# Performance work log

Measured on AMD Instinct MI355X. Metric: run time of the kernel, lower is better.

Reference implementation:

```python
import jax, jax.numpy as jnp
import numpy as np

B, P, L = 1024, 20, 3          # batch pairs, paths per pair, path length
T = L + 2                      # LSTM sequence length (news1 + path + news2)
E = 128                        # embedding_size (compressed / LSTM hidden)
D_DOC = 768                    # doc_embedding_size
D_ENT = 100                    # entity_embedding_size
N_DOC, N_ENT, N_REL = 50000, 200000, 60
GAMMA = 2.0
EPS = 1e-7


def setup_inputs() -> dict:
    key = jax.random.key(0)
    ks = jax.random.split(key, 24)
    s = lambda fan_in: 1.0 / np.sqrt(fan_in)
    u = lambda k, shape, sc: jax.random.uniform(k, shape, jnp.float32, -sc, sc)
    return {
        "item1": jax.random.randint(ks[0], (B,), 0, N_DOC),
        "item2": jax.random.randint(ks[1], (B,), 0, N_DOC),
        "paths": jax.random.randint(ks[2], (B, P, L), 0, N_ENT),
        "edges": jax.random.randint(ks[3], (B, P, L), 0, N_REL),
        "label": jnp.round(jax.random.uniform(ks[4], (B,), jnp.float32)),
        # embedding tables (frozen pretrained in the original)
        "doc_table": jax.random.normal(ks[5], (N_DOC, D_DOC), jnp.float32),
        "entity_table": jax.random.normal(ks[6], (N_ENT, D_ENT), jnp.float32),
        "relation_table": jax.random.normal(ks[7], (N_REL, D_ENT), jnp.float32),
        # news_compress: Linear(D_DOC,E) -> ELU -> Linear(E,E) -> Tanh
        "nc_W1": u(ks[8], (D_DOC, E), s(D_DOC)), "nc_b1": u(ks[9], (E,), s(D_DOC)),
        "nc_W2": u(ks[10], (E, E), s(E)),        "nc_b2": u(ks[11], (E,), s(E)),
        # entity / relation compress: Linear(D_ENT,E) -> Tanh
        "ec_W": u(ks[12], (D_ENT, E), s(D_ENT)), "ec_b": u(ks[13], (E,), s(D_ENT)),
        "rc_W": u(ks[14], (D_ENT, E), s(D_ENT)), "rc_b": u(ks[15], (E,), s(D_ENT)),
        # LSTM(input=2E, hidden=E); torch gate order i,f,g,o
        "W_ih": u(ks[16], (4 * E, 2 * E), s(E)), "W_hh": u(ks[17], (4 * E, E), s(E)),
        "b_ih": u(ks[18], (4 * E,), s(E)),       "b_hh": u(ks[19], (4 * E,), s(E)),
        # mlp: Linear(E,E) -> ReLU -> Linear(E,1)
        "mlp_W1": u(ks[20], (E, E), s(E)), "mlp_b1": u(ks[21], (E,), s(E)),
        "mlp_W2": u(ks[22], (E, 1), s(E)), "mlp_b2": u(ks[23], (1,), s(E)),
    }


def _lstm_last(x, W_ih, W_hh, b_ih, b_hh):
    # x: [N, T, 2E] -> last hidden state [N, E]
    N = x.shape[0]
    H = W_hh.shape[1]
    b = b_ih + b_hh

    def step(carry, xt):
        h, c = carry
        gates = xt @ W_ih.T + h @ W_hh.T + b          # [N, 4H]
        i, f, g, o = jnp.split(gates, 4, axis=-1)
        c = jax.nn.sigmoid(f) * c + jax.nn.sigmoid(i) * jnp.tanh(g)
        h = jax.nn.sigmoid(o) * jnp.tanh(c)
        return (h, c), None

    init = (jnp.zeros((N, H), x.dtype), jnp.zeros((N, H), x.dtype))
    (h, _), _ = jax.lax.scan(step, init, jnp.swapaxes(x, 0, 1))  # scan over T
    return h


def reference(item1, item2, paths, edges, label,
              doc_table, entity_table, relation_table,
              nc_W1, nc_b1, nc_W2, nc_b2, ec_W, ec_b, rc_W, rc_b,
              W_ih, W_hh, b_ih, b_hh, mlp_W1, mlp_b1, mlp_W2, mlp_b2):
    news_compress = lambda d: jnp.tanh(jax.nn.elu(d @ nc_W1 + nc_b1) @ nc_W2 + nc_b2)
    news1 = news_compress(doc_table[item1])               # [B, E]
    news2 = news_compress(doc_table[item2])               # [B, E]

    node_emb = jnp.tanh(entity_table[paths] @ ec_W + ec_b)          # [B,P,L,E]
    edge_ids = jnp.concatenate([edges, jnp.zeros((B, P, 2), edges.dtype)], axis=-1)  # edge+[0,0]
    rel_emb = jnp.tanh(relation_table[edge_ids] @ rc_W + rc_b)      # [B,P,T,E]

    n1 = jnp.broadcast_to(news1[:, None, None, :], (B, P, 1, E))
    n2 = jnp.broadcast_to(news2[:, None, None, :], (B, P, 1, E))
    nodes_seq = jnp.concatenate([n1, node_emb, n2], axis=2)         # [B,P,T,E]
    lstm_in = jnp.concatenate([nodes_seq, rel_emb], axis=-1)        # [B,P,T,2E]

    h_last = _lstm_last(lstm_in.reshape(B * P, T, 2 * E), W_ih, W_hh, b_ih, b_hh)
    scores = (jax.nn.relu(h_last @ mlp_W1 + mlp_b1) @ mlp_W2 + mlp_b2).reshape(B, P)

    predicts = jax.nn.sigmoid(jax.nn.logsumexp(scores / GAMMA, axis=1))  # [B]
    p = jnp.clip(predicts, EPS, 1.0 - EPS)
    loss = -jnp.mean(label * jnp.log(p) + (1.0 - label) * jnp.log(1.0 - p))
    return loss, predicts, scores
```

## Files before the change

### kernel.cpp

```cpp
#include <hip/hip_runtime.h>
#include <hip/hip_bf16.h>

#define B_  1024
#define P_  20
#define L_  3
#define T_  5
#define E_  128
#define N_  (B_*P_)
#define DDOC 768
#define DENT 100
#define XROWS 124929

typedef unsigned short u16;
typedef unsigned int   u32;
typedef __attribute__((ext_vector_type(8))) __bf16 bf16x8;
typedef __attribute__((ext_vector_type(4))) float  f32x4;

__device__ __forceinline__ float sigmoidf_(float x) { return 1.f / (1.f + expf(-x)); }
__device__ __forceinline__ u16 f2bf_rne(float x) {
    u32 b = __float_as_uint(x);
    b += 0x7fffu + ((b >> 16) & 1u);
    return (u16)(b >> 16);
}
__device__ __forceinline__ float bf2f(u16 u) { return __uint_as_float(((u32)u) << 16); }
__device__ __forceinline__ u32 pack2(u16 a, u16 b) { return (u32)a | ((u32)b << 16); }

__global__ __launch_bounds__(256) void news_kernel(
    const int* __restrict__ item1, const int* __restrict__ item2,
    const float* __restrict__ doc_table,
    const float* __restrict__ W1, const float* __restrict__ b1,
    const float* __restrict__ W2, const float* __restrict__ b2,
    u16* __restrict__ xh, u16* __restrict__ xl)
{
    __shared__ float d_lds[8][DDOC];
    __shared__ float h1_lds[8][132];
    const int tid = threadIdx.x;
    const int row0 = blockIdx.x * 8;

    for (int i = tid; i < 8 * 192; i += 256) {
        int r = i / 192, q = i % 192;
        int gr = row0 + r;
        int id = (gr < B_) ? item1[gr] : item2[gr - B_];
        reinterpret_cast<float4*>(&d_lds[r][0])[q] =
            reinterpret_cast<const float4*>(doc_table + (size_t)id * DDOC)[q];
    }
    __syncthreads();

    const int tn = tid & 127;
    const int tm = tid >> 7;
    float acc[4];
#pragma unroll
    for (int r = 0; r < 4; r++) acc[r] = b1[tn];

    for (int k = 0; k < DDOC; k += 4) {
        float w0 = W1[(k + 0) * 128 + tn];
        float w1 = W1[(k + 1) * 128 + tn];
        float w2 = W1[(k + 2) * 128 + tn];
        float w3 = W1[(k + 3) * 128 + tn];
#pragma unroll
        for (int r = 0; r < 4; r++) {
            const float4 dv = *reinterpret_cast<const float4*>(&d_lds[tm * 4 + r][k]);
            acc[r] = fmaf(dv.x, w0, acc[r]);
            acc[r] = fmaf(dv.y, w1, acc[r]);
            acc[r] = fmaf(dv.z, w2, acc[r]);
            acc[r] = fmaf(dv.w, w3, acc[r]);
        }
    }
#pragma unroll
    for (int r = 0; r < 4; r++) {
        float v = acc[r];
        h1_lds[tm * 4 + r][tn] = (v > 0.f) ? v : expm1f(v);
    }
    __syncthreads();

    float acc2[4];
#pragma unroll
    for (int r = 0; r < 4; r++) acc2[r] = b2[tn];
    for (int k = 0; k < 128; k += 4) {
        float w0 = W2[(k + 0) * 128 + tn];
        float w1 = W2[(k + 1) * 128 + tn];
        float w2 = W2[(k + 2) * 128 + tn];
        float w3 = W2[(k + 3) * 128 + tn];
#pragma unroll
        for (int r = 0; r < 4; r++) {
            const float4 hv = *reinterpret_cast<const float4*>(&h1_lds[tm * 4 + r][k]);
            acc2[r] = fmaf(hv.x, w0, acc2[r]);
            acc2[r] = fmaf(hv.y, w1, acc2[r]);
            acc2[r] = fmaf(hv.z, w2, acc2[r]);
            acc2[r] = fmaf(hv.w, w3, acc2[r]);
        }
    }
#pragma unroll
    for (int r = 0; r < 4; r++) {
        float v = tanhf(acc2[r]);
        size_t off = (size_t)(row0 + tm * 4 + r) * 128 + tn;
        u16 hh = f2bf_rne(v);
        xh[off] = hh;
        xl[off] = f2bf_rne(v - bf2f(hh));
    }
}

__global__ __launch_bounds__(256) void compress_kernel(
    const int* __restrict__ paths, const int* __restrict__ edges,
    const float* __restrict__ entity_table, const float* __restrict__ relation_table,
    const float* __restrict__ ec_W, const float* __restrict__ ec_b,
    const float* __restrict__ rc_W, const float* __restrict__ rc_b,
    u16* __restrict__ xh, u16* __restrict__ xl)
{
    __shared__ float w_lds[DENT][128];
    __shared__ float x_lds[32][104];
    __shared__ int idx_lds[32];

    const int tid = threadIdx.x;
    const int bid = blockIdx.x;
    const bool is_ent  = (bid < 1920);
    const bool is_rel0 = (bid == 3840);
    const float* W     = is_ent ? ec_W : rc_W;
    const float* bias  = is_ent ? ec_b : rc_b;
    const float* table = is_ent ? entity_table : relation_table;
    int nrows; int row0; int xbase;
    if (is_ent)        { row0 = bid * 32;          nrows = 32; xbase = 2048; }
    else if (!is_rel0) { row0 = (bid - 1920) * 32; nrows = 32; xbase = 63488; }
    else               { row0 = 0;                 nrows = 1;  xbase = 124928; }

    for (int i = tid; i < 3200; i += 256)
        reinterpret_cast<float4*>(&w_lds[0][0])[i] = reinterpret_cast<const float4*>(W)[i];
    if (tid < nrows) {
        int gr = row0 + tid;
        idx_lds[tid] = is_rel0 ? 0 : (is_ent ? paths[gr] : edges[gr]);
    }
    __syncthreads();

    for (int i = tid; i < nrows * 25; i += 256) {
        int r = i / 25, q = i % 25;
        reinterpret_cast<float4*>(&x_lds[r][0])[q] =
            reinterpret_cast<const float4*>(table + (size_t)idx_lds[r] * DENT)[q];
    }
    __syncthreads();

    const int tn = tid & 31;
    const int tm = tid >> 5;
    float acc[4][4];
#pragma unroll
    for (int ri = 0; ri < 4; ri++)
#pragma unroll
        for (int cj = 0; cj < 4; cj++) acc[ri][cj] = bias[tn * 4 + cj];

    for (int k = 0; k < DENT; k += 4) {
        float4 wv[4];
#pragma unroll
        for (int kk = 0; kk < 4; kk++)
            wv[kk] = *reinterpret_cast<const float4*>(&w_lds[k + kk][tn * 4]);
#pragma unroll
        for (int ri = 0; ri < 4; ri++) {
            const float4 xv = *reinterpret_cast<const float4*>(&x_lds[tm * 4 + ri][k]);
            float xs[4] = {xv.x, xv.y, xv.z, xv.w};
#pragma unroll
            for (int kk = 0; kk < 4; kk++) {
                acc[ri][0] = fmaf(xs[kk], wv[kk].x, acc[ri][0]);
                acc[ri][1] = fmaf(xs[kk], wv[kk].y, acc[ri][1]);
                acc[ri][2] = fmaf(xs[kk], wv[kk].z, acc[ri][2]);
                acc[ri][3] = fmaf(xs[kk], wv[kk].w, acc[ri][3]);
            }
        }
    }
#pragma unroll
    for (int ri = 0; ri < 4; ri++) {
        int r = tm * 4 + ri;
        if (r < nrows) {
            size_t xrow = (size_t)(xbase + row0 + r);
            u16 hh[4], ll[4];
#pragma unroll
            for (int cj = 0; cj < 4; cj++) {
                float v = tanhf(acc[ri][cj]);
                hh[cj] = f2bf_rne(v);
                ll[cj] = f2bf_rne(v - bf2f(hh[cj]));
            }
            uint2 oh, ol;
            oh.x = pack2(hh[0], hh[1]); oh.y = pack2(hh[2], hh[3]);
            ol.x = pack2(ll[0], ll[1]); ol.y = pack2(ll[2], ll[3]);
            *reinterpret_cast<uint2*>(&xh[xrow * 128 + tn * 4]) = oh;
            *reinterpret_cast<uint2*>(&xl[xrow * 128 + tn * 4]) = ol;
        }
    }
}

__global__ __launch_bounds__(256) void split_w_kernel(
    const float* __restrict__ W_ih, const float* __restrict__ W_hh,
    u16* __restrict__ wih_h, u16* __restrict__ wih_l,
    u16* __restrict__ whh_h, u16* __restrict__ whh_l)
{
    int i = blockIdx.x * 256 + threadIdx.x;
    if (i < 512 * 256) {
        float w = W_ih[i];
        u16 h = f2bf_rne(w);
        wih_h[i] = h; wih_l[i] = f2bf_rne(w - bf2f(h));
    } else {
        int j = i - 512 * 256;
        float w = W_hh[j];
        u16 h = f2bf_rne(w);
        whh_h[j] = h; whh_l[j] = f2bf_rne(w - bf2f(h));
    }
}

__global__ __launch_bounds__(256) void lstm_gemm(
    int t,
    const u16* __restrict__ xh, const u16* __restrict__ xl,
    const u16* __restrict__ wih_h, const u16* __restrict__ wih_l,
    const u16* __restrict__ whh_h, const u16* __restrict__ whh_l,
    const u16* __restrict__ h_hi, const u16* __restrict__ h_lo,
    float* __restrict__ gbuf)
{
    __shared__ u16 a_h[128 * 40], a_l[128 * 40], b_h[128 * 40], b_l[128 * 40];
    __shared__ int nrow[128], rrow[128];

    const int tid  = threadIdx.x;
    const int rb   = blockIdx.x >> 2;
    const int cb   = blockIdx.x & 3;
    const int row0 = rb * 128;
    const int gate0 = cb * 128;

    if (tid < 128) {
        int n = row0 + tid;
        int nr;
        if (t == 0)      nr = n / P_;
        else if (t == 4) nr = 1024 + n / P_;
        else             nr = 2048 + n * 3 + (t - 1);
        nrow[tid] = nr;
        rrow[tid] = (t < 3) ? (63488 + n * 3 + t) : 124928;
    }

    f32x4 acc[4][4];
#pragma unroll
    for (int rg = 0; rg < 4; rg++)
#pragma unroll
        for (int cg = 0; cg < 4; cg++)
            acc[rg][cg] = (f32x4){0.f, 0.f, 0.f, 0.f};

    const int ln   = tid & 63;
    const int wv   = tid >> 6;
    const int wrow = (wv >> 1) * 64;
    const int wcol = (wv & 1) * 64;
    const int l15  = ln & 15;
    const int lk   = (ln >> 4) * 8;

    const int nch = (t == 0) ? 8 : 12;
    __syncthreads();

    for (int ch = 0; ch < nch; ch++) {
        const int k0 = ch * 32;
        for (int i = tid; i < 2048; i += 256) {
            const int ab = i >> 10;
            const int pl = (i >> 9) & 1;
            const int r  = (i >> 2) & 127;
            const int q  = i & 3;
            const u16* src;
            if (ab == 0) {
                if (k0 < 128)
                    src = (pl ? xl : xh) + (size_t)nrow[r] * 128 + k0 + q * 8;
                else if (k0 < 256)
                    src = (pl ? xl : xh) + (size_t)rrow[r] * 128 + (k0 - 128) + q * 8;
                else
                    src = (pl ? h_lo : h_hi) + (size_t)(row0 + r) * 128 + (k0 - 256) + q * 8;
            } else {
                if (k0 < 256)
                    src = (pl ? wih_l : wih_h) + (size_t)(gate0 + r) * 256 + k0 + q * 8;
                else
                    src = (pl ? whh_l : whh_h) + (size_t)(gate0 + r) * 128 + (k0 - 256) + q * 8;
            }
            u16* dst = (ab ? (pl ? b_l : b_h) : (pl ? a_l : a_h)) + r * 40 + q * 8;
            *reinterpret_cast<uint4*>(dst) = *reinterpret_cast<const uint4*>(src);
        }
        __syncthreads();

        bf16x8 ah[4], al[4], bh[4], bl[4];
#pragma unroll
        for (int g = 0; g < 4; g++) {
            const int ao = (wrow + g * 16 + l15) * 40 + lk;
            ah[g] = *reinterpret_cast<const bf16x8*>(&a_h[ao]);
            al[g] = *reinterpret_cast<const bf16x8*>(&a_l[ao]);
            const int bo = (wcol + g * 16 + l15) * 40 + lk;
            bh[g] = *reinterpret_cast<const bf16x8*>(&b_h[bo]);
            bl[g] = *reinterpret_cast<const bf16x8*>(&b_l[bo]);
        }
#pragma unroll
        for (int rg = 0; rg < 4; rg++)
#pragma unroll
            for (int cg = 0; cg < 4; cg++) {
                acc[rg][cg] = __builtin_amdgcn_mfma_f32_16x16x32_bf16(ah[rg], bh[cg], acc[rg][cg], 0, 0, 0);
                acc[rg][cg] = __builtin_amdgcn_mfma_f32_16x16x32_bf16(al[rg], bh[cg], acc[rg][cg], 0, 0, 0);
                acc[rg][cg] = __builtin_amdgcn_mfma_f32_16x16x32_bf16(ah[rg], bl[cg], acc[rg][cg], 0, 0, 0);
            }
        __syncthreads();
    }

#pragma unroll
    for (int rg = 0; rg < 4; rg++)
#pragma unroll
        for (int cg = 0; cg < 4; cg++) {
            const int col = gate0 + wcol + cg * 16 + l15;
#pragma unroll
            for (int e = 0; e < 4; e++) {
                const int row = row0 + wrow + rg * 16 + (ln >> 4) * 4 + e;
                gbuf[(size_t)row * 512 + col] = acc[rg][cg][e];
            }
        }
}

__global__ __launch_bounds__(256) void cell_kernel(
    int t,
    const float* __restrict__ gbuf,
    const float* __restrict__ b_ih, const float* __restrict__ b_hh,
    float* __restrict__ cbuf,
    u16* __restrict__ h_hi, u16* __restrict__ h_lo)
{
    const int idx = blockIdx.x * 256 + threadIdx.x;
    const int n  = idx >> 7;
    const int hd = idx & 127;
    const size_t base = (size_t)n * 512 + hd;
    float gi = gbuf[base +   0] + b_ih[hd +   0] + b_hh[hd +   0];
    float gf = gbuf[base + 128] + b_ih[hd + 128] + b_hh[hd + 128];
    float gg = gbuf[base + 256] + b_ih[hd + 256] + b_hh[hd + 256];
    float go = gbuf[base + 384] + b_ih[hd + 384] + b_hh[hd + 384];
    float cp = (t == 0) ? 0.f : cbuf[idx];
    float cn = sigmoidf_(gf) * cp + sigmoidf_(gi) * tanhf(gg);
    cbuf[idx] = cn;
    float hn = sigmoidf_(go) * tanhf(cn);
    u16 hh = f2bf_rne(hn);
    h_hi[idx] = hh;
    h_lo[idx] = f2bf_rne(hn - bf2f(hh));
}

__global__ __launch_bounds__(256) void mlp_kernel(
    const u16* __restrict__ h_hi, const u16* __restrict__ h_lo,
    const float* __restrict__ W1, const float* __restrict__ b1,
    const float* __restrict__ W2, const float* __restrict__ b2,
    float* __restrict__ scores)
{
    __shared__ float h_lds[16][132];
    __shared__ float z_lds[16][132];
    const int tid = threadIdx.x;
    const int row0 = blockIdx.x * 16;

    {
        const int r = tid >> 4, q = tid & 15;
        const size_t off = (size_t)(row0 + r) * 128 + q * 8;
        uint4 vh = *reinterpret_cast<const uint4*>(&h_hi[off]);
        uint4 vl = *reinterpret_cast<const uint4*>(&h_lo[off]);
        const u16* sh = reinterpret_cast<const u16*>(&vh);
        const u16* sl = reinterpret_cast<const u16*>(&vl);
#pragma unroll
        for (int e = 0; e < 8; e++)
            h_lds[r][q * 8 + e] = bf2f(sh[e]) + bf2f(sl[e]);
    }
    __syncthreads();

    const int tn = tid & 127;
    const int tm = tid >> 7;
    float acc[8];
#pragma unroll
    for (int r = 0; r < 8; r++) acc[r] = b1[tn];
    for (int k = 0; k < 128; k += 4) {
        float w0 = W1[(k + 0) * 128 + tn];
        float w1 = W1[(k + 1) * 128 + tn];
        float w2 = W1[(k + 2) * 128 + tn];
        float w3 = W1[(k + 3) * 128 + tn];
#pragma unroll
        for (int r = 0; r < 8; r++) {
            const float4 hv = *reinterpret_cast<const float4*>(&h_lds[tm * 8 + r][k]);
            acc[r] = fmaf(hv.x, w0, acc[r]);
            acc[r] = fmaf(hv.y, w1, acc[r]);
            acc[r] = fmaf(hv.z, w2, acc[r]);
            acc[r] = fmaf(hv.w, w3, acc[r]);
        }
    }
#pragma unroll
    for (int r = 0; r < 8; r++)
        z_lds[tm * 8 + r][tn] = fmaxf(acc[r], 0.f);
    __syncthreads();

    const int row = tid >> 4;
    const int part = tid & 15;
    float s = 0.f;
#pragma unroll
    for (int i = 0; i < 8; i++) {
        int j = part + i * 16;
        s += z_lds[row][j] * W2[j];
    }
    s += __shfl_xor(s, 8, 16);
    s += __shfl_xor(s, 4, 16);
    s += __shfl_xor(s, 2, 16);
    s += __shfl_xor(s, 1, 16);
    if (part == 0)
        scores[row0 + row] = s + b2[0];
}

__global__ __launch_bounds__(1024) void final_kernel(
    const float* __restrict__ label, const float* scores, float* out)
{
    __shared__ float red[1024];
    const int b = threadIdx.x;
    const float* s = scores + (size_t)b * P_;
    float m = -1e30f;
#pragma unroll
    for (int p = 0; p < P_; p++) m = fmaxf(m, s[p] * 0.5f);
    float sum = 0.f;
#pragma unroll
    for (int p = 0; p < P_; p++) sum += expf(s[p] * 0.5f - m);
    float lse = m + logf(sum);
    float pr = 1.f / (1.f + expf(-lse));
    out[1 + b] = pr;
    float pc = fminf(fmaxf(pr, 1e-7f), 1.f - 1e-7f);
    float lb = label[b];
    red[b] = -(lb * logf(pc) + (1.f - lb) * logf(1.f - pc));
    __syncthreads();
    for (int st = 512; st > 0; st >>= 1) {
        if (b < st) red[b] += red[b + st];
        __syncthreads();
    }
    if (b == 0) out[0] = red[0] * (1.f / 1024.f);
}

extern "C" void kernel_launch(void* const* d_in, const int* in_sizes, int n_in,
                              void* d_out, int out_size, void* d_ws, size_t ws_size,
                              hipStream_t stream)
{
    const int*   item1     = (const int*)  d_in[0];
    const int*   item2     = (const int*)  d_in[1];
    const int*   paths     = (const int*)  d_in[2];
    const int*   edges     = (const int*)  d_in[3];
    const float* label     = (const float*)d_in[4];
    const float* doc_table = (const float*)d_in[5];
    const float* ent_table = (const float*)d_in[6];
    const float* rel_table = (const float*)d_in[7];
    const float* nc_W1     = (const float*)d_in[8];
    const float* nc_b1     = (const float*)d_in[9];
    const float* nc_W2     = (const float*)d_in[10];
    const float* nc_b2     = (const float*)d_in[11];
    const float* ec_W      = (const float*)d_in[12];
    const float* ec_b      = (const float*)d_in[13];
    const float* rc_W      = (const float*)d_in[14];
    const float* rc_b      = (const float*)d_in[15];
    const float* W_ih      = (const float*)d_in[16];
    const float* W_hh      = (const float*)d_in[17];
    const float* b_ih      = (const float*)d_in[18];
    const float* b_hh      = (const float*)d_in[19];
    const float* mlp_W1    = (const float*)d_in[20];
    const float* mlp_b1    = (const float*)d_in[21];
    const float* mlp_W2    = (const float*)d_in[22];
    const float* mlp_b2    = (const float*)d_in[23];

    char* p = (char*)d_ws;
    u16* xh    = (u16*)p;  p += (size_t)XROWS * 128 * 2;
    u16* xl    = (u16*)p;  p += (size_t)XROWS * 128 * 2;
    u16* wih_h = (u16*)p;  p += 512 * 256 * 2;
    u16* wih_l = (u16*)p;  p += 512 * 256 * 2;
    u16* whh_h = (u16*)p;  p += 512 * 128 * 2;
    u16* whh_l = (u16*)p;  p += 512 * 128 * 2;
    float* gbuf = (float*)p; p += (size_t)N_ * 512 * 4;
    float* cbuf = (float*)p; p += (size_t)N_ * 128 * 4;
    u16* h_hi  = (u16*)p;  p += (size_t)N_ * 128 * 2;
    u16* h_lo  = (u16*)p;  p += (size_t)N_ * 128 * 2;

    float* out    = (float*)d_out;
    float* scores = out + 1 + B_;

    news_kernel<<<256, 256, 0, stream>>>(item1, item2, doc_table,
                                         nc_W1, nc_b1, nc_W2, nc_b2, xh, xl);
    compress_kernel<<<3841, 256, 0, stream>>>(paths, edges, ent_table, rel_table,
                                              ec_W, ec_b, rc_W, rc_b, xh, xl);
    split_w_kernel<<<768, 256, 0, stream>>>(W_ih, W_hh, wih_h, wih_l, whh_h, whh_l);

    for (int t = 0; t < T_; t++) {
        lstm_gemm<<<640, 256, 0, stream>>>(t, xh, xl, wih_h, wih_l, whh_h, whh_l,
                                           h_hi, h_lo, gbuf);
        cell_kernel<<<N_ * 128 / 256, 256, 0, stream>>>(t, gbuf, b_ih, b_hh,
                                                        cbuf, h_hi, h_lo);
    }
    mlp_kernel<<<1280, 256, 0, stream>>>(h_hi, h_lo, mlp_W1, mlp_b1, mlp_W2, mlp_b2, scores);
    final_kernel<<<1, 1024, 0, stream>>>(label, scores, out);
}
```

Baseline: 715.4 us.

## Compress relation table once, MFMA entity compress, async double-buffered LSTM GEMM loads

Relation embeddings are now compressed only for the 60 distinct relation ids, and the LSTM GEMM gathers them through the edge indices. This replaces the per-path relation rows and shrinks the x buffer. Entity compression moves from scalar FP32 FMAs to split-bf16 MFMA, using transposed weights prepared in a merged prep kernel. The LSTM GEMM now loads tiles straight from global memory into XOR-swizzled LDS with double buffering and explicit waitcnt/barrier control, so loads overlap with MFMA work. The hand-placed waitcnt and barrier ordering raises the risk of subtle synchronisation bugs.

```diff
diff --git a/kernel.cpp b/kernel.cpp
--- a/kernel.cpp
+++ b/kernel.cpp
@@ -9,7 +9,9 @@
 #define N_  (B_*P_)
 #define DDOC 768
 #define DENT 100
-#define XROWS 124929
+#define NODE_BASE 2048
+#define RELC_BASE 63488
+#define XROWS 63548
 
 typedef unsigned short u16;
 typedef unsigned int   u32;
@@ -24,6 +26,12 @@
 }
 __device__ __forceinline__ float bf2f(u16 u) { return __uint_as_float(((u32)u) << 16); }
 __device__ __forceinline__ u32 pack2(u16 a, u16 b) { return (u32)a | ((u32)b << 16); }
+
+__device__ __forceinline__ void gl2lds16(const void* g, void* l) {
+    __builtin_amdgcn_global_load_lds(
+        (const __attribute__((address_space(1))) void*)g,
+        (__attribute__((address_space(3))) void*)l, 16, 0, 0);
+}
 
 __global__ __launch_bounds__(256) void news_kernel(
     const int* __restrict__ item1, const int* __restrict__ item2,
@@ -100,106 +108,183 @@
     }
 }
 
-__global__ __launch_bounds__(256) void compress_kernel(
-    const int* __restrict__ paths, const int* __restrict__ edges,
-    const float* __restrict__ entity_table, const float* __restrict__ relation_table,
-    const float* __restrict__ ec_W, const float* __restrict__ ec_b,
-    const float* __restrict__ rc_W, const float* __restrict__ rc_b,
-    u16* __restrict__ xh, u16* __restrict__ xl)
-{
-    __shared__ float w_lds[DENT][128];
-    __shared__ float x_lds[32][104];
-    __shared__ int idx_lds[32];
-
-    const int tid = threadIdx.x;
-    const int bid = blockIdx.x;
-    const bool is_ent  = (bid < 1920);
-    const bool is_rel0 = (bid == 3840);
-    const float* W     = is_ent ? ec_W : rc_W;
-    const float* bias  = is_ent ? ec_b : rc_b;
-    const float* table = is_ent ? entity_table : relation_table;
-    int nrows; int row0; int xbase;
-    if (is_ent)        { row0 = bid * 32;          nrows = 32; xbase = 2048; }
-    else if (!is_rel0) { row0 = (bid - 1920) * 32; nrows = 32; xbase = 63488; }
-    else               { row0 = 0;                 nrows = 1;  xbase = 124928; }
-
-    for (int i = tid; i < 3200; i += 256)
-        reinterpret_cast<float4*>(&w_lds[0][0])[i] = reinterpret_cast<const float4*>(W)[i];
-    if (tid < nrows) {
-        int gr = row0 + tid;
-        idx_lds[tid] = is_rel0 ? 0 : (is_ent ? paths[gr] : edges[gr]);
-    }
-    __syncthreads();
-
-    for (int i = tid; i < nrows * 25; i += 256) {
-        int r = i / 25, q = i % 25;
-        reinterpret_cast<float4*>(&x_lds[r][0])[q] =
-            reinterpret_cast<const float4*>(table + (size_t)idx_lds[r] * DENT)[q];
-    }
-    __syncthreads();
-
-    const int tn = tid & 31;
-    const int tm = tid >> 5;
-    float acc[4][4];
-#pragma unroll
-    for (int ri = 0; ri < 4; ri++)
-#pragma unroll
-        for (int cj = 0; cj < 4; cj++) acc[ri][cj] = bias[tn * 4 + cj];
-
-    for (int k = 0; k < DENT; k += 4) {
-        float4 wv[4];
-#pragma unroll
-        for (int kk = 0; kk < 4; kk++)
-            wv[kk] = *reinterpret_cast<const float4*>(&w_lds[k + kk][tn * 4]);
-#pragma unroll
-        for (int ri = 0; ri < 4; ri++) {
-            const float4 xv = *reinterpret_cast<const float4*>(&x_lds[tm * 4 + ri][k]);
-            float xs[4] = {xv.x, xv.y, xv.z, xv.w};
-#pragma unroll
-            for (int kk = 0; kk < 4; kk++) {
-                acc[ri][0] = fmaf(xs[kk], wv[kk].x, acc[ri][0]);
-                acc[ri][1] = fmaf(xs[kk], wv[kk].y, acc[ri][1]);
-                acc[ri][2] = fmaf(xs[kk], wv[kk].z, acc[ri][2]);
-                acc[ri][3] = fmaf(xs[kk], wv[kk].w, acc[ri][3]);
-            }
-        }
-    }
-#pragma unroll
-    for (int ri = 0; ri < 4; ri++) {
-        int r = tm * 4 + ri;
-        if (r < nrows) {
-            size_t xrow = (size_t)(xbase + row0 + r);
-            u16 hh[4], ll[4];
-#pragma unroll
-            for (int cj = 0; cj < 4; cj++) {
-                float v = tanhf(acc[ri][cj]);
-                hh[cj] = f2bf_rne(v);
-                ll[cj] = f2bf_rne(v - bf2f(hh[cj]));
-            }
-            uint2 oh, ol;
-            oh.x = pack2(hh[0], hh[1]); oh.y = pack2(hh[2], hh[3]);
-            ol.x = pack2(ll[0], ll[1]); ol.y = pack2(ll[2], ll[3]);
-            *reinterpret_cast<uint2*>(&xh[xrow * 128 + tn * 4]) = oh;
-            *reinterpret_cast<uint2*>(&xl[xrow * 128 + tn * 4]) = ol;
-        }
-    }
-}
-
-__global__ __launch_bounds__(256) void split_w_kernel(
+__global__ __launch_bounds__(256) void prep_kernel(
     const float* __restrict__ W_ih, const float* __restrict__ W_hh,
+    const float* __restrict__ ec_W, const float* __restrict__ rc_W,
     u16* __restrict__ wih_h, u16* __restrict__ wih_l,
-    u16* __restrict__ whh_h, u16* __restrict__ whh_l)
+    u16* __restrict__ whh_h, u16* __restrict__ whh_l,
+    u16* __restrict__ ecwt_h, u16* __restrict__ ecwt_l,
+    u16* __restrict__ rcwt_h, u16* __restrict__ rcwt_l)
 {
     int i = blockIdx.x * 256 + threadIdx.x;
-    if (i < 512 * 256) {
+    if (i < 131072) {
         float w = W_ih[i];
         u16 h = f2bf_rne(w);
         wih_h[i] = h; wih_l[i] = f2bf_rne(w - bf2f(h));
-    } else {
-        int j = i - 512 * 256;
+    } else if (i < 196608) {
+        int j = i - 131072;
         float w = W_hh[j];
         u16 h = f2bf_rne(w);
         whh_h[j] = h; whh_l[j] = f2bf_rne(w - bf2f(h));
+    } else if (i < 212992) {
+        int j = i - 196608;
+        int col = j & 127, k = j >> 7;
+        float w = (k < DENT) ? ec_W[k * 128 + col] : 0.f;
+        u16 h = f2bf_rne(w);
+        ecwt_h[col * 128 + k] = h; ecwt_l[col * 128 + k] = f2bf_rne(w - bf2f(h));
+    } else {
+        int j = i - 212992;
+        int col = j & 127, k = j >> 7;
+        float w = (k < DENT) ? rc_W[k * 128 + col] : 0.f;
+        u16 h = f2bf_rne(w);
+        rcwt_h[col * 128 + k] = h; rcwt_l[col * 128 + k] = f2bf_rne(w - bf2f(h));
+    }
+}
+
+__global__ __launch_bounds__(256) void compress_mfma(
+    const int* __restrict__ paths,
+    const float* __restrict__ entity_table, const float* __restrict__ relation_table,
+    const u16* __restrict__ ecwt_h, const u16* __restrict__ ecwt_l,
+    const u16* __restrict__ rcwt_h, const u16* __restrict__ rcwt_l,
+    const float* __restrict__ ec_b, const float* __restrict__ rc_b,
+    u16* __restrict__ xh, u16* __restrict__ xl)
+{
+    __shared__ char lds_raw[65536];
+    u16* a_lds = (u16*)lds_raw;
+    u16* b_lds = (u16*)(lds_raw + 18432);
+    u32* o_lds = (u32*)lds_raw;
+
+    const int tid = threadIdx.x;
+    const int bid = blockIdx.x;
+    const bool is_rel = (bid == 480);
+    const int r0 = bid * 128;
+    const u16* wth = is_rel ? rcwt_h : ecwt_h;
+    const u16* wtl = is_rel ? rcwt_l : ecwt_l;
+    const float* bias = is_rel ? rc_b : ec_b;
+    const float* table = is_rel ? relation_table : entity_table;
+
+    const int ar = tid >> 1, ahalf = tid & 1;
+    int gidx;
+    if (is_rel) gidx = (ar < 60) ? ar : 0;
+    else        gidx = paths[r0 + ar];
+    const float* arow = table + (size_t)gidx * DENT;
+
+    const int ln = tid & 63, wv = tid >> 6;
+    const int wrow = (wv >> 1) * 64, wcol = (wv & 1) * 64;
+    const int l15 = ln & 15, lq = ln >> 4;
+
+    f32x4 acc[4][4];
+#pragma unroll
+    for (int cg = 0; cg < 4; cg++) {
+        float bv = bias[wcol + cg * 16 + l15];
+#pragma unroll
+        for (int rg = 0; rg < 4; rg++)
+            acc[rg][cg] = (f32x4){bv, bv, bv, bv};
+    }
+
+    for (int c = 0; c < 4; ++c) {
+        {
+            float v[16];
+#pragma unroll
+            for (int q = 0; q < 4; ++q) {
+                int kq = c * 32 + ahalf * 16 + q * 4;
+                float4 f = (kq < DENT) ? *reinterpret_cast<const float4*>(arow + kq)
+                                       : make_float4(0.f, 0.f, 0.f, 0.f);
+                v[q * 4 + 0] = f.x; v[q * 4 + 1] = f.y;
+                v[q * 4 + 2] = f.z; v[q * 4 + 3] = f.w;
+            }
+            u16 hh[16], llo[16];
+#pragma unroll
+            for (int e = 0; e < 16; ++e) {
+                hh[e] = f2bf_rne(v[e]);
+                llo[e] = f2bf_rne(v[e] - bf2f(hh[e]));
+            }
+            u16* ap = a_lds + ar * 72;
+            uint4 o0, o1, o2, o3;
+            o0.x = pack2(hh[0], hh[1]);  o0.y = pack2(hh[2], hh[3]);
+            o0.z = pack2(hh[4], hh[5]);  o0.w = pack2(hh[6], hh[7]);
+            o1.x = pack2(hh[8], hh[9]);  o1.y = pack2(hh[10], hh[11]);
+            o1.z = pack2(hh[12], hh[13]); o1.w = pack2(hh[14], hh[15]);
+            o2.x = pack2(llo[0], llo[1]);  o2.y = pack2(llo[2], llo[3]);
+            o2.z = pack2(llo[4], llo[5]);  o2.w = pack2(llo[6], llo[7]);
+            o3.x = pack2(llo[8], llo[9]);  o3.y = pack2(llo[10], llo[11]);
+            o3.z = pack2(llo[12], llo[13]); o3.w = pack2(llo[14], llo[15]);
+            *reinterpret_cast<uint4*>(ap + ahalf * 16 + 0) = o0;
+            *reinterpret_cast<uint4*>(ap + ahalf * 16 + 8) = o1;
+            *reinterpret_cast<uint4*>(ap + 32 + ahalf * 16 + 0) = o2;
+            *reinterpret_cast<uint4*>(ap + 32 + ahalf * 16 + 8) = o3;
+        }
+#pragma unroll
+        for (int i = 0; i < 4; ++i) {
+            int idx = tid + i * 256;
+            int br = idx >> 3, s = idx & 7;
+            const u16* src = ((s & 4) ? wtl : wth) + br * 128 + c * 32 + (s & 3) * 8;
+            *reinterpret_cast<uint4*>(b_lds + br * 72 + s * 8) =
+                *reinterpret_cast<const uint4*>(src);
+        }
+        __syncthreads();
+
+        bf16x8 ah[4], al[4], bh[4], bl[4];
+#pragma unroll
+        for (int g = 0; g < 4; ++g) {
+            const u16* ap = a_lds + (wrow + g * 16 + l15) * 72 + lq * 8;
+            ah[g] = *reinterpret_cast<const bf16x8*>(ap);
+            al[g] = *reinterpret_cast<const bf16x8*>(ap + 32);
+            const u16* bp = b_lds + (wcol + g * 16 + l15) * 72 + lq * 8;
+            bh[g] = *reinterpret_cast<const bf16x8*>(bp);
+            bl[g] = *reinterpret_cast<const bf16x8*>(bp + 32);
+        }
+#pragma unroll
+        for (int rg = 0; rg < 4; rg++)
+#pragma unroll
+            for (int cg = 0; cg < 4; cg++) {
+                acc[rg][cg] = __builtin_amdgcn_mfma_f32_16x16x32_bf16(ah[rg], bh[cg], acc[rg][cg], 0, 0, 0);
+                acc[rg][cg] = __builtin_amdgcn_mfma_f32_16x16x32_bf16(al[rg], bh[cg], acc[rg][cg], 0, 0, 0);
+                acc[rg][cg] = __builtin_amdgcn_mfma_f32_16x16x32_bf16(ah[rg], bl[cg], acc[rg][cg], 0, 0, 0);
+            }
+        __syncthreads();
+    }
+
+#pragma unroll
+    for (int rg = 0; rg < 4; rg++)
+#pragma unroll
+        for (int cg = 0; cg < 4; cg++) {
+            const int col = wcol + cg * 16 + l15;
+#pragma unroll
+            for (int e = 0; e < 4; ++e) {
+                const int row = wrow + rg * 16 + lq * 4 + e;
+                float tv = tanhf(acc[rg][cg][e]);
+                u16 th = f2bf_rne(tv);
+                u16 tl = f2bf_rne(tv - bf2f(th));
+                o_lds[row * 128 + col] = pack2(th, tl);
+            }
+        }
+    __syncthreads();
+#pragma unroll
+    for (int i = 0; i < 8; ++i) {
+        int idx = tid + i * 256;
+        int row = idx >> 4, oct = idx & 15;
+        int xr;
+        if (is_rel) {
+            if (row >= 60) continue;
+            xr = RELC_BASE + row;
+        } else {
+            xr = NODE_BASE + r0 + row;
+        }
+        u32 w[8];
+#pragma unroll
+        for (int j = 0; j < 8; ++j) w[j] = o_lds[row * 128 + oct * 8 + j];
+        uint4 hv, lv;
+        hv.x = (w[0] & 0xffffu) | (w[1] << 16);
+        hv.y = (w[2] & 0xffffu) | (w[3] << 16);
+        hv.z = (w[4] & 0xffffu) | (w[5] << 16);
+        hv.w = (w[6] & 0xffffu) | (w[7] << 16);
+        lv.x = (w[0] >> 16) | (w[1] & 0xffff0000u);
+        lv.y = (w[2] >> 16) | (w[3] & 0xffff0000u);
+        lv.z = (w[4] >> 16) | (w[5] & 0xffff0000u);
+        lv.w = (w[6] >> 16) | (w[7] & 0xffff0000u);
+        *reinterpret_cast<uint4*>(xh + (size_t)xr * 128 + oct * 8) = hv;
+        *reinterpret_cast<uint4*>(xl + (size_t)xr * 128 + oct * 8) = lv;
     }
 }
 
@@ -209,10 +294,11 @@
     const u16* __restrict__ wih_h, const u16* __restrict__ wih_l,
     const u16* __restrict__ whh_h, const u16* __restrict__ whh_l,
     const u16* __restrict__ h_hi, const u16* __restrict__ h_lo,
+    const int* __restrict__ edges,
     float* __restrict__ gbuf)
 {
-    __shared__ u16 a_h[128 * 40], a_l[128 * 40], b_h[128 * 40], b_l[128 * 40];
-    __shared__ int nrow[128], rrow[128];
+    __shared__ u16 lds_a[2 * 8192];
+    __shared__ u16 lds_b[2 * 8192];
 
     const int tid  = threadIdx.x;
     const int rb   = blockIdx.x >> 2;
@@ -220,14 +306,33 @@
     const int row0 = rb * 128;
     const int gate0 = cb * 128;
 
-    if (tid < 128) {
-        int n = row0 + tid;
+    const int ln = tid & 63, wv = tid >> 6;
+    const int wrow = (wv >> 1) * 64, wcol = (wv & 1) * 64;
+    const int l15 = ln & 15, lq = ln >> 4;
+
+    const int lr8 = ln >> 3;
+    const int sphys = ln & 7;
+    const int slog = sphys ^ lr8;
+    const bool plo = (slog & 4) != 0;
+    const int koff = (slog & 3) * 8;
+
+    const u16* nb[4]; const u16* rbp[4]; const u16* hb[4];
+    const u16* wb_ih[4]; const u16* wb_hh[4];
+#pragma unroll
+    for (int j = 0; j < 4; ++j) {
+        const int r = 32 * wv + 8 * j + lr8;
+        const int n = row0 + r;
         int nr;
         if (t == 0)      nr = n / P_;
         else if (t == 4) nr = 1024 + n / P_;
-        else             nr = 2048 + n * 3 + (t - 1);
-        nrow[tid] = nr;
-        rrow[tid] = (t < 3) ? (63488 + n * 3 + t) : 124928;
+        else             nr = NODE_BASE + n * 3 + (t - 1);
+        nb[j] = (plo ? xl : xh) + (size_t)nr * 128 + koff;
+        const int rr = RELC_BASE + ((t < 3) ? edges[n * 3 + t] : 0);
+        rbp[j] = (plo ? xl : xh) + (size_t)rr * 128 + koff;
+        hb[j] = (plo ? h_lo : h_hi) + (size_t)n * 128 + koff;
+        const int gr = gate0 + r;
+        wb_ih[j] = (plo ? wih_l : wih_h) + (size_t)gr * 256 + koff;
+        wb_hh[j] = (plo ? whh_l : whh_h) + (size_t)gr * 128 + koff;
     }
 
     f32x4 acc[4][4];
@@ -237,51 +342,52 @@
         for (int cg = 0; cg < 4; cg++)
             acc[rg][cg] = (f32x4){0.f, 0.f, 0.f, 0.f};
 
-    const int ln   = tid & 63;
-    const int wv   = tid >> 6;
-    const int wrow = (wv >> 1) * 64;
-    const int wcol = (wv & 1) * 64;
-    const int l15  = ln & 15;
-    const int lk   = (ln >> 4) * 8;
-
     const int nch = (t == 0) ? 8 : 12;
-    __syncthreads();
-
-    for (int ch = 0; ch < nch; ch++) {
-        const int k0 = ch * 32;
-        for (int i = tid; i < 2048; i += 256) {
-            const int ab = i >> 10;
-            const int pl = (i >> 9) & 1;
-            const int r  = (i >> 2) & 127;
-            const int q  = i & 3;
-            const u16* src;
-            if (ab == 0) {
-                if (k0 < 128)
-                    src = (pl ? xl : xh) + (size_t)nrow[r] * 128 + k0 + q * 8;
-                else if (k0 < 256)
-                    src = (pl ? xl : xh) + (size_t)rrow[r] * 128 + (k0 - 128) + q * 8;
-                else
-                    src = (pl ? h_lo : h_hi) + (size_t)(row0 + r) * 128 + (k0 - 256) + q * 8;
-            } else {
-                if (k0 < 256)
-                    src = (pl ? wih_l : wih_h) + (size_t)(gate0 + r) * 256 + k0 + q * 8;
-                else
-                    src = (pl ? whh_l : whh_h) + (size_t)(gate0 + r) * 128 + (k0 - 256) + q * 8;
-            }
-            u16* dst = (ab ? (pl ? b_l : b_h) : (pl ? a_l : a_h)) + r * 40 + q * 8;
-            *reinterpret_cast<uint4*>(dst) = *reinterpret_cast<const uint4*>(src);
-        }
-        __syncthreads();
-
+
+    auto STAGE = [&](int c, int kb) {
+        u16* ab = lds_a + kb * 8192;
+        u16* bb = lds_b + kb * 8192;
+#pragma unroll
+        for (int j = 0; j < 4; ++j) {
+            const u16* s;
+            if (c < 4)      s = nb[j] + c * 32;
+            else if (c < 8) s = rbp[j] + (c - 4) * 32;
+            else            s = hb[j] + (c - 8) * 32;
+            gl2lds16(s, ab + (32 * wv + 8 * j) * 64);
+        }
+#pragma unroll
+        for (int j = 0; j < 4; ++j) {
+            const u16* s = (c < 8) ? (wb_ih[j] + c * 32) : (wb_hh[j] + (c - 8) * 32);
+            gl2lds16(s, bb + (32 * wv + 8 * j) * 64);
+        }
+    };
+
+    STAGE(0, 0);
+    for (int c = 0; c < nch; ++c) {
+        const int kb = c & 1;
+        if (c + 1 < nch) {
+            STAGE(c + 1, kb ^ 1);
+            __builtin_amdgcn_sched_barrier(0);
+            asm volatile("s_waitcnt vmcnt(8)" ::: "memory");
+        } else {
+            asm volatile("s_waitcnt vmcnt(0)" ::: "memory");
+        }
+        __builtin_amdgcn_s_barrier();
+        __builtin_amdgcn_sched_barrier(0);
+
+        const u16* ab = lds_a + kb * 8192;
+        const u16* bb = lds_b + kb * 8192;
         bf16x8 ah[4], al[4], bh[4], bl[4];
 #pragma unroll
-        for (int g = 0; g < 4; g++) {
-            const int ao = (wrow + g * 16 + l15) * 40 + lk;
-            ah[g] = *reinterpret_cast<const bf16x8*>(&a_h[ao]);
-            al[g] = *reinterpret_cast<const bf16x8*>(&a_l[ao]);
-            const int bo = (wcol + g * 16 + l15) * 40 + lk;
-            bh[g] = *reinterpret_cast<const bf16x8*>(&b_h[bo]);
-            bl[g] = *reinterpret_cast<const bf16x8*>(&b_l[bo]);
+        for (int g = 0; g < 4; ++g) {
+            const int r = wrow + g * 16 + l15;
+            const u16* ap = ab + r * 64;
+            ah[g] = *reinterpret_cast<const bf16x8*>(ap + ((lq    ) ^ (r & 7)) * 8);
+            al[g] = *reinterpret_cast<const bf16x8*>(ap + ((lq + 4) ^ (r & 7)) * 8);
+            const int rc = wcol + g * 16 + l15;
+            const u16* bp = bb + rc * 64;
+            bh[g] = *reinterpret_cast<const bf16x8*>(bp + ((lq    ) ^ (rc & 7)) * 8);
+            bl[g] = *reinterpret_cast<const bf16x8*>(bp + ((lq + 4) ^ (rc & 7)) * 8);
         }
 #pragma unroll
         for (int rg = 0; rg < 4; rg++)
@@ -291,7 +397,9 @@
                 acc[rg][cg] = __builtin_amdgcn_mfma_f32_16x16x32_bf16(al[rg], bh[cg], acc[rg][cg], 0, 0, 0);
                 acc[rg][cg] = __builtin_amdgcn_mfma_f32_16x16x32_bf16(ah[rg], bl[cg], acc[rg][cg], 0, 0, 0);
             }
-        __syncthreads();
+        asm volatile("s_waitcnt lgkmcnt(0)" ::: "memory");
+        __builtin_amdgcn_s_barrier();
+        __builtin_amdgcn_sched_barrier(0);
     }
 
 #pragma unroll
@@ -301,7 +409,7 @@
             const int col = gate0 + wcol + cg * 16 + l15;
 #pragma unroll
             for (int e = 0; e < 4; e++) {
-                const int row = row0 + wrow + rg * 16 + (ln >> 4) * 4 + e;
+                const int row = row0 + wrow + rg * 16 + lq * 4 + e;
                 gbuf[(size_t)row * 512 + col] = acc[rg][cg][e];
             }
         }
@@ -451,29 +559,35 @@
     const float* mlp_b2    = (const float*)d_in[23];
 
     char* p = (char*)d_ws;
-    u16* xh    = (u16*)p;  p += (size_t)XROWS * 128 * 2;
-    u16* xl    = (u16*)p;  p += (size_t)XROWS * 128 * 2;
-    u16* wih_h = (u16*)p;  p += 512 * 256 * 2;
-    u16* wih_l = (u16*)p;  p += 512 * 256 * 2;
-    u16* whh_h = (u16*)p;  p += 512 * 128 * 2;
-    u16* whh_l = (u16*)p;  p += 512 * 128 * 2;
+    u16* xh     = (u16*)p;  p += (size_t)XROWS * 128 * 2;
+    u16* xl     = (u16*)p;  p += (size_t)XROWS * 128 * 2;
+    u16* wih_h  = (u16*)p;  p += 131072 * 2;
+    u16* wih_l  = (u16*)p;  p += 131072 * 2;
+    u16* whh_h  = (u16*)p;  p += 65536 * 2;
+    u16* whh_l  = (u16*)p;  p += 65536 * 2;
+    u16* ecwt_h = (u16*)p;  p += 16384 * 2;
+    u16* ecwt_l = (u16*)p;  p += 16384 * 2;
+    u16* rcwt_h = (u16*)p;  p += 16384 * 2;
+    u16* rcwt_l = (u16*)p;  p += 16384 * 2;
     float* gbuf = (float*)p; p += (size_t)N_ * 512 * 4;
     float* cbuf = (float*)p; p += (size_t)N_ * 128 * 4;
-    u16* h_hi  = (u16*)p;  p += (size_t)N_ * 128 * 2;
-    u16* h_lo  = (u16*)p;  p += (size_t)N_ * 128 * 2;
+    u16* h_hi   = (u16*)p;  p += (size_t)N_ * 128 * 2;
+    u16* h_lo   = (u16*)p;  p += (size_t)N_ * 128 * 2;
 
     float* out    = (float*)d_out;
     float* scores = out + 1 + B_;
 
     news_kernel<<<256, 256, 0, stream>>>(item1, item2, doc_table,
                                          nc_W1, nc_b1, nc_W2, nc_b2, xh, xl);
-    compress_kernel<<<3841, 256, 0, stream>>>(paths, edges, ent_table, rel_table,
-                                              ec_W, ec_b, rc_W, rc_b, xh, xl);
-    split_w_kernel<<<768, 256, 0, stream>>>(W_ih, W_hh, wih_h, wih_l, whh_h, whh_l);
-
+    prep_kernel<<<896, 256, 0, stream>>>(W_ih, W_hh, ec_W, rc_W,
+                                         wih_h, wih_l, whh_h, whh_l,
+                                         ecwt_h, ecwt_l, rcwt_h, rcwt_l);
+    compress_mfma<<<481, 256, 0, stream>>>(paths, ent_table, rel_table,
+                                           ecwt_h, ecwt_l, rcwt_h, rcwt_l,
+                                           ec_b, rc_b, xh, xl);
     for (int t = 0; t < T_; t++) {
         lstm_gemm<<<640, 256, 0, stream>>>(t, xh, xl, wih_h, wih_l, whh_h, whh_l,
-                                           h_hi, h_lo, gbuf);
+                                           h_hi, h_lo, edges, gbuf);
         cell_kernel<<<N_ * 128 / 256, 256, 0, stream>>>(t, gbuf, b_ih, b_hh,
                                                         cbuf, h_hi, h_lo);
     }
```

After: 583.7 us. 18.4% less time.
